# Performance work log

Hardware: AMD Instinct MI355X
Metric: run time of the kernel (lower is better)

The kernel has to match this reference:

```python
import jax, jax.numpy as jnp
import numpy as np

B, L, D_IN, D_OUT, H = 8, 1024, 1024, 1024, 16
DH = D_OUT // H                      # 64
SCALE = 1.0 / float(np.sqrt(D_OUT // 2))  # 1/sqrt(512), matches buffer 'scale'
LAMBDA_INIT = 0.8 - 0.6 * float(np.exp(-0.3 * (1 - 1)))  # layer=1 -> 0.2


def _rmsnorm(x, w):
    eps = jnp.finfo(x.dtype).eps
    return x * jax.lax.rsqrt(jnp.mean(x * x, axis=-1, keepdims=True) + eps) * w


def _orth(key, shape):
    a = jax.random.normal(key, shape, dtype=jnp.float32)
    q, r = jnp.linalg.qr(a)
    return q * jnp.sign(jnp.diagonal(r))


def setup_inputs() -> dict:
    key = jax.random.key(0)
    ks = jax.random.split(key, 12)
    return {
        "x": jax.random.normal(ks[0], (B, L, D_IN), dtype=jnp.float32),
        "Wq": _orth(ks[1], (D_OUT, D_IN)), "bq": jnp.zeros((D_OUT,), jnp.float32),
        "Wk": _orth(ks[2], (D_OUT, D_IN)), "bk": jnp.zeros((D_OUT,), jnp.float32),
        "Wv": _orth(ks[3], (D_OUT, D_IN)), "bv": jnp.zeros((D_OUT,), jnp.float32),
        "lambda_params": jnp.full((4,), 0.8, jnp.float32),
        "g1": jnp.ones((D_IN,), jnp.float32),
        "g2": jnp.ones((DH,), jnp.float32),
        "g3": jnp.ones((D_OUT,), jnp.float32),
        "Wf1": _orth(ks[4], (D_OUT, D_OUT)), "bf1": jnp.zeros((D_OUT,), jnp.float32),
        "Wf2": _orth(ks[5], (D_OUT, D_OUT)), "bf2": jnp.zeros((D_OUT,), jnp.float32),
    }


def reference(x, Wq, bq, Wk, bk, Wv, bv, lambda_params, g1, g2, g3, Wf1, bf1, Wf2, bf2):
    xn = _rmsnorm(x, g1)                                   # [B,L,D_in]
    Q = (xn @ Wq.T + bq).reshape(B, L, H, DH)
    K = (xn @ Wk.T + bk).reshape(B, L, H, DH)
    V = (xn @ Wv.T + bv).reshape(B, L, H, DH)
    Q1, Q2 = jnp.split(Q, 2, axis=-1)                      # [B,L,H,DH/2]
    K1, K2 = jnp.split(K, 2, axis=-1)
    phi = jax.nn.elu
    # faithful to source: matmuls on last two dims of [B,L,H,*] -> contract heads per position
    kv1 = SCALE * jnp.einsum('blhd,blhe->blde', phi(K1), V)  # [B,L,DH/2,DH]
    kv2 = SCALE * jnp.einsum('blhd,blhe->blde', phi(K2), V)
    a1 = jnp.einsum('blhd,blde->blhe', phi(Q1), kv1)         # [B,L,H,DH]
    a2 = jnp.einsum('blhd,blde->blhe', phi(Q2), kv2)
    e0 = jnp.exp(lambda_params[0] * lambda_params[1])
    e1 = jnp.exp(lambda_params[2] * lambda_params[3])
    lmbda = e0 - e1 + LAMBDA_INIT
    attn = a1 - lmbda * a2                                  # inverse=False
    attn = (1.0 - LAMBDA_INIT) * _rmsnorm(attn, g2)
    attn = attn.reshape(B, L, D_OUT)
    attn = _rmsnorm(attn, g3) + attn
    h = jax.nn.gelu(attn @ Wf1.T + bf1, approximate=False)  # dropout=0 (eval)
    out = (h @ Wf2.T + bf2) + attn
    return out
```

## Files before the change

### kernel.cpp

```cpp
#include <hip/hip_runtime.h>
#include <cmath>

typedef __bf16 bf16_t;
typedef __attribute__((ext_vector_type(8))) __bf16 bf16x8;
typedef __attribute__((ext_vector_type(4))) __bf16 bf16x4;
typedef __attribute__((ext_vector_type(4))) float f32x4;

#define RMS_EPS 1.1920929e-07f
#define KV_SCALE 0.04419417382415922f

__device__ __forceinline__ void gload16(const void* g, void* l) {
  __builtin_amdgcn_global_load_lds((const __attribute__((address_space(1))) void*)g,
                                   (__attribute__((address_space(3))) void*)l, 16, 0, 0);
}

__global__ __launch_bounds__(256) void cast_bf16_1m(const float* __restrict__ s,
                                                    bf16_t* __restrict__ d) {
  int i = (blockIdx.x * 256 + threadIdx.x) * 4;
  float4 v = *(const float4*)(s + i);
  bf16x4 o;
  o[0] = (bf16_t)v.x; o[1] = (bf16_t)v.y; o[2] = (bf16_t)v.z; o[3] = (bf16_t)v.w;
  *(bf16x4*)(d + i) = o;
}

__global__ void concat_bias(const float* __restrict__ bq, const float* __restrict__ bk,
                            const float* __restrict__ bv, float* __restrict__ dst) {
  int i = blockIdx.x * 256 + threadIdx.x;
  float v;
  if (i < 1024) v = bq[i];
  else if (i < 2048) v = bk[i - 1024];
  else v = bv[i - 2048];
  dst[i] = v;
}

__global__ __launch_bounds__(256) void rmsnorm_x(const float* __restrict__ x,
                                                 const float* __restrict__ g,
                                                 bf16_t* __restrict__ xn) {
  const int m = blockIdx.x, t = threadIdx.x;
  const float4 v = ((const float4*)(x + (size_t)m * 1024))[t];
  float ss = v.x * v.x + v.y * v.y + v.z * v.z + v.w * v.w;
  #pragma unroll
  for (int o = 1; o < 64; o <<= 1) ss += __shfl_xor(ss, o);
  __shared__ float red[4];
  if ((t & 63) == 0) red[t >> 6] = ss;
  __syncthreads();
  const float r = rsqrtf((red[0] + red[1] + red[2] + red[3]) * (1.f / 1024.f) + RMS_EPS);
  const float4 gv = ((const float4*)g)[t];
  bf16x4 o;
  o[0] = (bf16_t)(v.x * r * gv.x); o[1] = (bf16_t)(v.y * r * gv.y);
  o[2] = (bf16_t)(v.z * r * gv.z); o[3] = (bf16_t)(v.w * r * gv.w);
  *(bf16x4*)(xn + (size_t)m * 1024 + t * 4) = o;
}

template <int MODE>
__global__ __launch_bounds__(256) void gemm_nt(const bf16_t* __restrict__ A,
                                               const bf16_t* __restrict__ Bm,
                                               const float* __restrict__ bias,
                                               const bf16_t* __restrict__ residb,
                                               void* __restrict__ outp,
                                               int M, int N, int K) {
  __shared__ bf16_t As[128][32];
  __shared__ bf16_t Bs[128][32];
  const int t = threadIdx.x;
  const int lane = t & 63;
  const int w = t >> 6;
  const int wm = w >> 1, wn = w & 1;
  const int nTN = N >> 7;

  const int nwg = gridDim.x;
  const int cpx = nwg >> 3;
  int bid = blockIdx.x;
  bid = (bid & 7) * cpx + (bid >> 3);
  const int tm = bid / nTN, tn = bid % nTN;

  const size_t rowA = (size_t)tm * 128;
  const size_t rowB = (size_t)tn * 128;
  const size_t sK = (size_t)K;

  f32x4 acc[4][4];
  #pragma unroll
  for (int i = 0; i < 4; ++i)
    #pragma unroll
    for (int j = 0; j < 4; ++j) acc[i][j] = (f32x4){0.f, 0.f, 0.f, 0.f};

  const int sr = lane >> 2;
  const int sc = (lane & 3) << 3;
  const int r16 = lane & 15;
  const int c8 = (lane >> 4) << 3;

  for (int k0 = 0; k0 < K; k0 += 32) {
    gload16(A  + (rowA +      w * 16 + sr) * sK + (k0 + sc), &As[w * 16][0]);
    gload16(A  + (rowA + 64 + w * 16 + sr) * sK + (k0 + sc), &As[64 + w * 16][0]);
    gload16(Bm + (rowB +      w * 16 + sr) * sK + (k0 + sc), &Bs[w * 16][0]);
    gload16(Bm + (rowB + 64 + w * 16 + sr) * sK + (k0 + sc), &Bs[64 + w * 16][0]);
    __syncthreads();

    bf16x8 a[4], b[4];
    #pragma unroll
    for (int i = 0; i < 4; ++i) {
      a[i] = *(const bf16x8*)&As[wm * 64 + i * 16 + r16][c8];
      b[i] = *(const bf16x8*)&Bs[wn * 64 + i * 16 + r16][c8];
    }
    #pragma unroll
    for (int i = 0; i < 4; ++i)
      #pragma unroll
      for (int j = 0; j < 4; ++j)
        acc[i][j] = __builtin_amdgcn_mfma_f32_16x16x32_bf16(a[i], b[j], acc[i][j], 0, 0, 0);
    __syncthreads();
  }

  const int hi4 = (lane >> 4) * 4;
  #pragma unroll
  for (int i = 0; i < 4; ++i) {
    #pragma unroll
    for (int j = 0; j < 4; ++j) {
      const int gc = tn * 128 + wn * 64 + j * 16 + r16;
      const float bv = bias[gc];
      #pragma unroll
      for (int r = 0; r < 4; ++r) {
        const int gr = tm * 128 + wm * 64 + i * 16 + hi4 + r;
        float v = acc[i][j][r] + bv;
        if constexpr (MODE == 0) {
          ((bf16_t*)outp)[(size_t)gr * N + gc] = (bf16_t)v;
        } else if constexpr (MODE == 1) {
          v = 0.5f * v * (1.0f + erff(v * 0.70710678118654752f));
          ((bf16_t*)outp)[(size_t)gr * N + gc] = (bf16_t)v;
        } else {
          v += (float)residb[(size_t)gr * N + gc];
          ((float*)outp)[(size_t)gr * N + gc] = v;
        }
      }
    }
  }
}

__global__ __launch_bounds__(256) void attn_fused(const bf16_t* __restrict__ qkv,
                                                  const float* __restrict__ lp,
                                                  const float* __restrict__ g2,
                                                  const float* __restrict__ g3,
                                                  bf16_t* __restrict__ attnb) {
  __shared__ __align__(16) char lds[4][6656];
  const int t = threadIdx.x;
  const int lane = t & 63;
  const int w = t >> 6;
  const int m = blockIdx.x * 4 + w;
  char* const sQ  = lds[w];
  char* const sK  = lds[w] + 2048;
  char* const sVt = lds[w] + 4096;
  char* const sSb = lds[w] + 6144;

  const float lmbda = __expf(lp[0] * lp[1]) - __expf(lp[2] * lp[3]) + 0.2f;
  const int l7 = lane & 7, l8 = lane >> 3;
  const bf16x8* src = (const bf16x8*)(qkv + (size_t)m * 3072);

  const float qsc = (l7 < 4) ? KV_SCALE : -lmbda * KV_SCALE;
  #pragma unroll
  for (int c = 0; c < 2; ++c) {
    bf16x8 v = src[c * 64 + lane];
    const int h = c * 8 + l8;
    bf16x8 o;
    #pragma unroll
    for (int i = 0; i < 8; ++i) {
      float f = (float)v[i];
      f = f > 0.f ? f : __expf(f) - 1.f;
      o[i] = (bf16_t)(f * qsc);
    }
    *(bf16x8*)(sQ + ((h * 128 + 16 * l7) ^ ((h & 7) << 4))) = o;
  }
  #pragma unroll
  for (int c = 2; c < 4; ++c) {
    bf16x8 v = src[c * 64 + lane];
    const int h = (c - 2) * 8 + l8;
    bf16x8 o;
    #pragma unroll
    for (int i = 0; i < 8; ++i) {
      float f = (float)v[i];
      f = f > 0.f ? f : __expf(f) - 1.f;
      o[i] = (bf16_t)f;
    }
    *(bf16x8*)(sK + ((h * 128 + 16 * l7) ^ ((h & 7) << 4))) = o;
  }
  #pragma unroll
  for (int c = 4; c < 6; ++c) {
    bf16x8 v = src[c * 64 + lane];
    const int h = (c - 4) * 8 + l8;
    #pragma unroll
    for (int i = 0; i < 8; ++i) {
      const int e = 8 * l7 + i;
      *(bf16_t*)(sVt + ((e * 32 + h * 2) ^ ((e & 1) << 4))) = v[i];
    }
  }

  const int r16 = lane & 15, g4 = lane >> 4;
  f32x4 accS = {};
  {
    const int ra = r16 * 128;
    const int sw = (r16 & 7) << 4;
    bf16x8 a0 = *(const bf16x8*)(sQ + ((ra + 16 * g4) ^ sw));
    bf16x8 b0 = *(const bf16x8*)(sK + ((ra + 16 * g4) ^ sw));
    bf16x8 a1 = *(const bf16x8*)(sQ + ((ra + 64 + 16 * g4) ^ sw));
    bf16x8 b1 = *(const bf16x8*)(sK + ((ra + 64 + 16 * g4) ^ sw));
    accS = __builtin_amdgcn_mfma_f32_16x16x32_bf16(a0, b0, accS, 0, 0, 0);
    accS = __builtin_amdgcn_mfma_f32_16x16x32_bf16(a1, b1, accS, 0, 0, 0);
  }

  #pragma unroll
  for (int r = 0; r < 4; ++r) {
    const int h = g4 * 4 + r;
    *(bf16_t*)(sSb + ((h * 32 + 2 * r16) ^ ((h & 1) << 4))) = (bf16_t)accS[r];
  }

  bf16x8 zf = {};
  bf16x8 aS = zf;
  if (lane < 32) aS = *(const bf16x8*)(sSb + ((r16 * 32 + 16 * g4) ^ ((r16 & 1) << 4)));
  f32x4 accA[4];
  #pragma unroll
  for (int j = 0; j < 4; ++j) {
    bf16x8 bV = zf;
    if (lane < 32) {
      const int row = j * 16 + r16;
      bV = *(const bf16x8*)(sVt + ((row * 32 + 16 * g4) ^ ((row & 1) << 4)));
    }
    f32x4 z4 = {};
    accA[j] = __builtin_amdgcn_mfma_f32_16x16x32_bf16(aS, bV, z4, 0, 0, 0);
  }

  float rnh[4];
  #pragma unroll
  for (int r = 0; r < 4; ++r) {
    float s = 0.f;
    #pragma unroll
    for (int j = 0; j < 4; ++j) s += accA[j][r] * accA[j][r];
    #pragma unroll
    for (int o = 1; o < 16; o <<= 1) s += __shfl_xor(s, o);
    rnh[r] = rsqrtf(s * (1.f / 64.f) + RMS_EPS);
  }
  float g2v[4];
  #pragma unroll
  for (int j = 0; j < 4; ++j) g2v[j] = g2[j * 16 + r16];
  float val[4][4];
  float tot = 0.f;
  #pragma unroll
  for (int j = 0; j < 4; ++j)
    #pragma unroll
    for (int r = 0; r < 4; ++r) {
      const float vv = accA[j][r] * rnh[r] * g2v[j] * 0.8f;
      val[j][r] = vv;
      tot += vv * vv;
    }
  #pragma unroll
  for (int o = 1; o < 64; o <<= 1) tot += __shfl_xor(tot, o);
  const float rn2 = rsqrtf(tot * (1.f / 1024.f) + RMS_EPS);

  bf16_t* dst = attnb + (size_t)m * 1024;
  #pragma unroll
  for (int j = 0; j < 4; ++j)
    #pragma unroll
    for (int r = 0; r < 4; ++r) {
      const int n = (g4 * 4 + r) * 64 + j * 16 + r16;
      const float ov = val[j][r] * rn2 * g3[n] + val[j][r];
      dst[n] = (bf16_t)ov;
    }
}

extern "C" void kernel_launch(void* const* d_in, const int* in_sizes, int n_in,
                              void* d_out, int out_size, void* d_ws, size_t ws_size,
                              hipStream_t stream) {
  const float* x   = (const float*)d_in[0];
  const float* Wq  = (const float*)d_in[1];
  const float* bq  = (const float*)d_in[2];
  const float* Wk  = (const float*)d_in[3];
  const float* bk  = (const float*)d_in[4];
  const float* Wv  = (const float*)d_in[5];
  const float* bv  = (const float*)d_in[6];
  const float* lp  = (const float*)d_in[7];
  const float* g1  = (const float*)d_in[8];
  const float* g2  = (const float*)d_in[9];
  const float* g3  = (const float*)d_in[10];
  const float* Wf1 = (const float*)d_in[11];
  const float* bf1 = (const float*)d_in[12];
  const float* Wf2 = (const float*)d_in[13];
  const float* bf2 = (const float*)d_in[14];

  char* ws = (char*)d_ws;
  bf16_t* wqkv  = (bf16_t*)(ws + 0);
  bf16_t* wf1b  = (bf16_t*)(ws + 6291456);
  bf16_t* wf2b  = (bf16_t*)(ws + 8388608);
  float*  bqkv  = (float*)(ws + 10485760);
  bf16_t* xn    = (bf16_t*)(ws + 10498048);
  bf16_t* qkv   = (bf16_t*)(ws + 27275264);
  bf16_t* attnb = (bf16_t*)(ws + 77606912);
  bf16_t* hbuf  = (bf16_t*)(ws + 94384128);

  cast_bf16_1m<<<1024, 256, 0, stream>>>(Wq, wqkv);
  cast_bf16_1m<<<1024, 256, 0, stream>>>(Wk, wqkv + (1u << 20));
  cast_bf16_1m<<<1024, 256, 0, stream>>>(Wv, wqkv + (2u << 20));
  cast_bf16_1m<<<1024, 256, 0, stream>>>(Wf1, wf1b);
  cast_bf16_1m<<<1024, 256, 0, stream>>>(Wf2, wf2b);
  concat_bias<<<12, 256, 0, stream>>>(bq, bk, bv, bqkv);
  rmsnorm_x<<<8192, 256, 0, stream>>>(x, g1, xn);
  gemm_nt<0><<<1536, 256, 0, stream>>>(xn, wqkv, bqkv, nullptr, (void*)qkv, 8192, 3072, 1024);
  attn_fused<<<2048, 256, 0, stream>>>(qkv, lp, g2, g3, attnb);
  gemm_nt<1><<<512, 256, 0, stream>>>(attnb, wf1b, bf1, nullptr, (void*)hbuf, 8192, 1024, 1024);
  gemm_nt<2><<<512, 256, 0, stream>>>(hbuf, wf2b, bf2, attnb, d_out, 8192, 1024, 1024);
}
```

Measured before the change: 283.4 us.

## Pipeline GEMMs with 4-stage LDS ring, larger tiles, and swizzle; fuse weight casts

```diff
diff --git a/kernel.cpp b/kernel.cpp
--- a/kernel.cpp
+++ b/kernel.cpp
@@ -14,13 +14,21 @@
                                    (__attribute__((address_space(3))) void*)l, 16, 0, 0);
 }
 
-__global__ __launch_bounds__(256) void cast_bf16_1m(const float* __restrict__ s,
-                                                    bf16_t* __restrict__ d) {
+__global__ __launch_bounds__(256) void cast_all(const float* __restrict__ s0,
+                                                const float* __restrict__ s1,
+                                                const float* __restrict__ s2,
+                                                const float* __restrict__ s3,
+                                                const float* __restrict__ s4,
+                                                bf16_t* __restrict__ d) {
+  const float* srcs[5] = {s0, s1, s2, s3, s4};
+  const int which = blockIdx.y;
+  const float* src = srcs[which];
+  bf16_t* dst = d + ((size_t)which << 20);
   int i = (blockIdx.x * 256 + threadIdx.x) * 4;
-  float4 v = *(const float4*)(s + i);
+  float4 v = *(const float4*)(src + i);
   bf16x4 o;
   o[0] = (bf16_t)v.x; o[1] = (bf16_t)v.y; o[2] = (bf16_t)v.z; o[3] = (bf16_t)v.w;
-  *(bf16x4*)(d + i) = o;
+  *(bf16x4*)(dst + i) = o;
 }
 
 __global__ void concat_bias(const float* __restrict__ bq, const float* __restrict__ bk,
@@ -53,19 +61,20 @@
 }
 
 template <int MODE>
-__global__ __launch_bounds__(256) void gemm_nt(const bf16_t* __restrict__ A,
-                                               const bf16_t* __restrict__ Bm,
-                                               const float* __restrict__ bias,
-                                               const bf16_t* __restrict__ residb,
-                                               void* __restrict__ outp,
-                                               int M, int N, int K) {
-  __shared__ bf16_t As[128][32];
-  __shared__ bf16_t Bs[128][32];
+__global__ __launch_bounds__(512, 2) void gemm2(const bf16_t* __restrict__ A,
+                                                const bf16_t* __restrict__ Bm,
+                                                const float* __restrict__ bias,
+                                                const bf16_t* __restrict__ residb,
+                                                void* __restrict__ outp,
+                                                int M, int N, int K) {
+  __shared__ bf16_t As[4][128][32];
+  __shared__ bf16_t Bs[4][256][32];
   const int t = threadIdx.x;
   const int lane = t & 63;
   const int w = t >> 6;
-  const int wm = w >> 1, wn = w & 1;
-  const int nTN = N >> 7;
+  const int wm = w >> 2;
+  const int wn = w & 3;
+  const int nTN = N >> 8;
 
   const int nwg = gridDim.x;
   const int cpx = nwg >> 3;
@@ -73,9 +82,25 @@
   bid = (bid & 7) * cpx + (bid >> 3);
   const int tm = bid / nTN, tn = bid % nTN;
 
-  const size_t rowA = (size_t)tm * 128;
-  const size_t rowB = (size_t)tn * 128;
   const size_t sK = (size_t)K;
+  const int NT = K >> 5;
+
+  const int sr = w * 16 + (lane >> 2);
+  const int ssw = (((lane & 3) ^ ((lane >> 2) & 3)) << 3);
+  const bf16_t* gA  = A  + ((size_t)tm * 128 + sr) * sK + ssw;
+  const bf16_t* gB0 = Bm + ((size_t)tn * 256 + sr) * sK + ssw;
+  const bf16_t* gB1 = gB0 + (size_t)128 * sK;
+
+  bf16_t* const AsF = &As[0][0][0];
+  bf16_t* const BsF = &Bs[0][0][0];
+  bf16_t* const dA  = &As[0][w * 16][0];
+  bf16_t* const dB0 = &Bs[0][w * 16][0];
+  bf16_t* const dB1 = &Bs[0][128 + w * 16][0];
+
+  const int r16 = lane & 15, g4 = lane >> 4;
+  const int scol = ((g4 ^ (r16 & 3)) << 3);
+  const int loA = (wm * 64 + r16) * 32 + scol;
+  const int loB = (wn * 64 + r16) * 32 + scol;
 
   f32x4 acc[4][4];
   #pragma unroll
@@ -83,43 +108,63 @@
     #pragma unroll
     for (int j = 0; j < 4; ++j) acc[i][j] = (f32x4){0.f, 0.f, 0.f, 0.f};
 
-  const int sr = lane >> 2;
-  const int sc = (lane & 3) << 3;
-  const int r16 = lane & 15;
-  const int c8 = (lane >> 4) << 3;
-
-  for (int k0 = 0; k0 < K; k0 += 32) {
-    gload16(A  + (rowA +      w * 16 + sr) * sK + (k0 + sc), &As[w * 16][0]);
-    gload16(A  + (rowA + 64 + w * 16 + sr) * sK + (k0 + sc), &As[64 + w * 16][0]);
-    gload16(Bm + (rowB +      w * 16 + sr) * sK + (k0 + sc), &Bs[w * 16][0]);
-    gload16(Bm + (rowB + 64 + w * 16 + sr) * sK + (k0 + sc), &Bs[64 + w * 16][0]);
+  auto STAGE = [&](int tt) {
+    const int sl = tt & 3;
+    const size_t ko = (size_t)tt << 5;
+    gload16(gA  + ko, dA  + sl * 4096);
+    gload16(gB0 + ko, dB0 + sl * 8192);
+    gload16(gB1 + ko, dB1 + sl * 8192);
+  };
+  auto READ = [&](int tt, bf16x8* aa, bf16x8* bb) {
+    const int sl = tt & 3;
+    const bf16_t* pa = AsF + sl * 4096 + loA;
+    const bf16_t* pb = BsF + sl * 8192 + loB;
+    aa[0] = *(const bf16x8*)(pa);        aa[1] = *(const bf16x8*)(pa + 512);
+    aa[2] = *(const bf16x8*)(pa + 1024); aa[3] = *(const bf16x8*)(pa + 1536);
+    bb[0] = *(const bf16x8*)(pb);        bb[1] = *(const bf16x8*)(pb + 512);
+    bb[2] = *(const bf16x8*)(pb + 1024); bb[3] = *(const bf16x8*)(pb + 1536);
+  };
+  auto BODY = [&](int tt, bf16x8* ca, bf16x8* cb, bf16x8* na, bf16x8* nb) {
+    if (tt + 4 <= NT) {
+      STAGE(tt + 3);
+      asm volatile("s_waitcnt vmcnt(6)" ::: "memory");
+    } else if (tt == NT - 3) {
+      asm volatile("s_waitcnt vmcnt(3)" ::: "memory");
+    } else if (tt == NT - 2) {
+      asm volatile("s_waitcnt vmcnt(0)" ::: "memory");
+    }
     __syncthreads();
-
-    bf16x8 a[4], b[4];
-    #pragma unroll
-    for (int i = 0; i < 4; ++i) {
-      a[i] = *(const bf16x8*)&As[wm * 64 + i * 16 + r16][c8];
-      b[i] = *(const bf16x8*)&Bs[wn * 64 + i * 16 + r16][c8];
-    }
-    #pragma unroll
-    for (int i = 0; i < 4; ++i)
+    if (tt + 1 < NT) READ(tt + 1, na, nb);
+    __builtin_amdgcn_s_setprio(1);
+    #pragma unroll
+    for (int mi = 0; mi < 4; ++mi)
       #pragma unroll
-      for (int j = 0; j < 4; ++j)
-        acc[i][j] = __builtin_amdgcn_mfma_f32_16x16x32_bf16(a[i], b[j], acc[i][j], 0, 0, 0);
-    __syncthreads();
-  }
-
-  const int hi4 = (lane >> 4) * 4;
-  #pragma unroll
-  for (int i = 0; i < 4; ++i) {
-    #pragma unroll
-    for (int j = 0; j < 4; ++j) {
-      const int gc = tn * 128 + wn * 64 + j * 16 + r16;
+      for (int nj = 0; nj < 4; ++nj)
+        acc[mi][nj] = __builtin_amdgcn_mfma_f32_16x16x32_bf16(ca[mi], cb[nj], acc[mi][nj], 0, 0, 0);
+    __builtin_amdgcn_s_setprio(0);
+  };
+
+  bf16x8 fa0[4], fb0[4], fa1[4], fb1[4];
+  STAGE(0); STAGE(1); STAGE(2);
+  asm volatile("s_waitcnt vmcnt(6)" ::: "memory");
+  __syncthreads();
+  READ(0, fa0, fb0);
+  for (int tt = 0; tt < NT; tt += 2) {
+    BODY(tt,     fa0, fb0, fa1, fb1);
+    BODY(tt + 1, fa1, fb1, fa0, fb0);
+  }
+
+  const int hi4 = g4 * 4;
+  #pragma unroll
+  for (int mi = 0; mi < 4; ++mi) {
+    #pragma unroll
+    for (int nj = 0; nj < 4; ++nj) {
+      const int gc = tn * 256 + wn * 64 + nj * 16 + r16;
       const float bv = bias[gc];
       #pragma unroll
       for (int r = 0; r < 4; ++r) {
-        const int gr = tm * 128 + wm * 64 + i * 16 + hi4 + r;
-        float v = acc[i][j][r] + bv;
+        const int gr = tm * 128 + wm * 64 + mi * 16 + hi4 + r;
+        float v = acc[mi][nj][r] + bv;
         if constexpr (MODE == 0) {
           ((bf16_t*)outp)[(size_t)gr * N + gc] = (bf16_t)v;
         } else if constexpr (MODE == 1) {
@@ -292,15 +337,11 @@
   bf16_t* attnb = (bf16_t*)(ws + 77606912);
   bf16_t* hbuf  = (bf16_t*)(ws + 94384128);
 
-  cast_bf16_1m<<<1024, 256, 0, stream>>>(Wq, wqkv);
-  cast_bf16_1m<<<1024, 256, 0, stream>>>(Wk, wqkv + (1u << 20));
-  cast_bf16_1m<<<1024, 256, 0, stream>>>(Wv, wqkv + (2u << 20));
-  cast_bf16_1m<<<1024, 256, 0, stream>>>(Wf1, wf1b);
-  cast_bf16_1m<<<1024, 256, 0, stream>>>(Wf2, wf2b);
+  cast_all<<<dim3(1024, 5), 256, 0, stream>>>(Wq, Wk, Wv, Wf1, Wf2, wqkv);
   concat_bias<<<12, 256, 0, stream>>>(bq, bk, bv, bqkv);
   rmsnorm_x<<<8192, 256, 0, stream>>>(x, g1, xn);
-  gemm_nt<0><<<1536, 256, 0, stream>>>(xn, wqkv, bqkv, nullptr, (void*)qkv, 8192, 3072, 1024);
+  gemm2<0><<<768, 512, 0, stream>>>(xn, wqkv, bqkv, nullptr, (void*)qkv, 8192, 3072, 1024);
   attn_fused<<<2048, 256, 0, stream>>>(qkv, lp, g2, g3, attnb);
-  gemm_nt<1><<<512, 256, 0, stream>>>(attnb, wf1b, bf1, nullptr, (void*)hbuf, 8192, 1024, 1024);
-  gemm_nt<2><<<512, 256, 0, stream>>>(hbuf, wf2b, bf2, attnb, d_out, 8192, 1024, 1024);
-}
+  gemm2<1><<<256, 512, 0, stream>>>(attnb, wf1b, bf1, nullptr, (void*)hbuf, 8192, 1024, 1024);
+  gemm2<2><<<256, 512, 0, stream>>>(hbuf, wf2b, bf2, attnb, d_out, 8192, 1024, 1024);
+}
```

Result: slower. 289.5 us (+2.1%).
